# Kernel tuning notes

Hardware: AMD Instinct MI355X
Metric: run time of the kernel (lower is better)

Reference implementation:

```python
import jax, jax.numpy as jnp
import numpy as np

N, C, H, W = 64, 128, 32, 32
EPS = 1e-5


def _layernorm_chw(x, w, b):
    # LayerNorm over normalized_shape=(C,H,W): last 3 dims
    mu = jnp.mean(x, axis=(1, 2, 3), keepdims=True)
    var = jnp.var(x, axis=(1, 2, 3), keepdims=True)
    return (x - mu) * jax.lax.rsqrt(var + EPS) * w[None] + b[None]


def _conv1x1(x, w, b):
    # x: [N,C,H,W], w: [Cout,Cin], b: [Cout]
    return jnp.einsum('oc,nchw->nohw', w, x) + b[None, :, None, None]


def setup_inputs() -> dict:
    key = jax.random.key(0)
    ks = jax.random.split(key, 12)
    d = {
        'query': jax.random.normal(ks[0], (N, C, H, W), jnp.float32),
        'key': jax.random.normal(ks[1], (N, C, H, W), jnp.float32),
        'value': jax.random.normal(ks[2], (N, C, H, W), jnp.float32),
        'ln1_w': jnp.ones((C, H, W), jnp.float32),
        'ln1_b': jnp.zeros((C, H, W), jnp.float32),
        'ln2_w': jnp.ones((C, H, W), jnp.float32),
        'ln2_b': jnp.zeros((C, H, W), jnp.float32),
        'ln3_w': jnp.ones((C, H, W), jnp.float32),
        'ln3_b': jnp.zeros((C, H, W), jnp.float32),
        'wq': jax.random.normal(ks[3], (C, C), jnp.float32) / np.sqrt(C),
        'bq': jnp.zeros((C,), jnp.float32),
        'wk': jax.random.normal(ks[4], (C, C), jnp.float32) / np.sqrt(C),
        'bk': jnp.zeros((C,), jnp.float32),
        'wv': jax.random.normal(ks[5], (C, C), jnp.float32) / np.sqrt(C),
        'bv': jnp.zeros((C,), jnp.float32),
    }
    return d


def reference(query, key, value, ln1_w, ln1_b, ln2_w, ln2_b, ln3_w, ln3_b,
              wq, bq, wk, bk, wv, bv):
    qn = _layernorm_chw(query, ln1_w, ln1_b)  # residual uses normalized query
    kn = _layernorm_chw(key, ln2_w, ln2_b)
    vn = _layernorm_chw(value, ln3_w, ln3_b)
    q = _conv1x1(qn, wq, bq).reshape(N, C, H * W)
    k = _conv1x1(kn, wk, bk).reshape(N, C, H * W)
    v = _conv1x1(vn, wv, bv).reshape(N, C, H * W)
    # attention[n,i,j] = sum_c k[n,c,i] q[n,c,j] / sqrt(C); softmax over i (dim=1)
    attn = jnp.einsum('nci,ncj->nij', k, q) / jnp.sqrt(jnp.float32(C))
    attn = jax.nn.softmax(attn, axis=1)
    out = jnp.einsum('nci,nij->ncj', v, attn).reshape(N, C, H, W)
    x = qn + out
    return x.reshape(N, -1)  # flatten(start_dim=1)
```

## Files before the change

kernel.cpp:

```cpp
#include <hip/hip_runtime.h>


#define NS 64
#define CD 128
#define SD 1024
#define MEL (CD*SD)
#define SCALE 0.08838834764831845f

typedef __attribute__((ext_vector_type(4))) float floatx4;
typedef __attribute__((ext_vector_type(8))) short short8;
typedef __attribute__((ext_vector_type(4))) short short4v;

typedef __attribute__((address_space(1))) const void global_cvoid;
typedef __attribute__((address_space(3))) void lds_void;

__device__ __forceinline__ void gl16(const void* g, void* l) {
  __builtin_amdgcn_global_load_lds((global_cvoid*)g, (lds_void*)l, 16, 0, 0);
}
__device__ __forceinline__ unsigned short f2bf(float f) {
  union { float f; unsigned int i; } v; v.f = f;
  unsigned int i = v.i;
  return (unsigned short)((i + 0x7fffu + ((i >> 16) & 1u)) >> 16);
}
__device__ __forceinline__ unsigned int pkbf(float lo, float hi) {
  unsigned int r;
  asm("v_cvt_pk_bf16_f32 %0, %1, %2" : "=v"(r) : "v"(lo), "v"(hi));
  return r;
}
__device__ __forceinline__ short8 ld8_bf16(const float* __restrict__ p) {
  floatx4 a = *(const floatx4*)p;
  floatx4 b = *(const floatx4*)(p + 4);
  short8 r;
  r[0] = (short)f2bf(a[0]); r[1] = (short)f2bf(a[1]);
  r[2] = (short)f2bf(a[2]); r[3] = (short)f2bf(a[3]);
  r[4] = (short)f2bf(b[0]); r[5] = (short)f2bf(b[1]);
  r[6] = (short)f2bf(b[2]); r[7] = (short)f2bf(b[3]);
  return r;
}
__device__ __forceinline__ floatx4 mfma16(short8 a, short8 b, floatx4 c) {
  return __builtin_amdgcn_mfma_f32_16x16x32_bf16(a, b, c, 0, 0, 0);
}

__global__ __launch_bounds__(256) void stats_kernel(
    const float* __restrict__ q, const float* __restrict__ k,
    const float* __restrict__ v, float* __restrict__ sums)
{
  int b = blockIdx.x;
  int tn = b >> 3, part = b & 7;
  int t = tn >> 6;
  const float* x = (t == 0 ? q : (t == 1 ? k : v))
                 + (size_t)(tn & 63) * MEL + part * (MEL / 8);
  float s1 = 0.f, s2 = 0.f;
#pragma unroll
  for (int it = 0; it < 16; ++it) {
    floatx4 u = *(const floatx4*)(x + it * 1024 + threadIdx.x * 4);
#pragma unroll
    for (int j = 0; j < 4; ++j) { float f = u[j]; s1 += f; s2 += f * f; }
  }
#pragma unroll
  for (int off = 32; off; off >>= 1) {
    s1 += __shfl_xor(s1, off, 64);
    s2 += __shfl_xor(s2, off, 64);
  }
  if ((threadIdx.x & 63) == 0) {
    atomicAdd(&sums[tn], s1);
    atomicAdd(&sums[192 + tn], s2);
  }
}

__global__ __launch_bounds__(512, 4) void proj_kernel(
  const float* __restrict__ k, const float* __restrict__ v,
  const float* __restrict__ l2w, const float* __restrict__ l2b,
  const float* __restrict__ l3w, const float* __restrict__ l3b,
  const float* __restrict__ wk, const float* __restrict__ bk,
  const float* __restrict__ wv, const float* __restrict__ bv,
  const float* __restrict__ sums,
  unsigned short* __restrict__ kT, unsigned short* __restrict__ vN)
{
  int n  = blockIdx.x, t = blockIdx.y, st = blockIdx.z;
  const float* x  = (t == 0 ? k : v) + (size_t)n * MEL;
  const float* lw = (t == 0 ? l2w : l3w);
  const float* lb = (t == 0 ? l2b : l3b);
  const float* W  = (t == 0 ? wk : wv);
  const float* Bs = (t == 0 ? bk : bv);

  float mu  = sums[(t + 1) * 64 + n] * (1.f / MEL);
  float var = sums[192 + (t + 1) * 64 + n] * (1.f / MEL) - mu * mu;
  float rs  = rsqrtf(var + 1e-5f);
  float a_ln = rs, b_ln = -mu * rs;

  __shared__ __align__(16) unsigned short Xt[128 * 136];

  int tid = threadIdx.x;
  int cb = tid & 15, sb = (tid >> 4) & 15, half = tid >> 8;
  int s0 = st * 128;

  unsigned int w32[8][2];
#pragma unroll
  for (int pr = 0; pr < 2; ++pr) {
    int c0 = cb * 8 + half * 4 + pr * 2;
    const float* xp0 = x  + (size_t)c0 * SD + s0 + sb * 8;
    const float* wp0 = lw + (size_t)c0 * SD + s0 + sb * 8;
    const float* bp0 = lb + (size_t)c0 * SD + s0 + sb * 8;
    float xv0[8], xv1[8], wv0[8], wv1[8], bv0[8], bv1[8];
    *(floatx4*)xv0 = *(const floatx4*)xp0;       *(floatx4*)(xv0+4) = *(const floatx4*)(xp0+4);
    *(floatx4*)xv1 = *(const floatx4*)(xp0+SD);  *(floatx4*)(xv1+4) = *(const floatx4*)(xp0+SD+4);
    *(floatx4*)wv0 = *(const floatx4*)wp0;       *(floatx4*)(wv0+4) = *(const floatx4*)(wp0+4);
    *(floatx4*)wv1 = *(const floatx4*)(wp0+SD);  *(floatx4*)(wv1+4) = *(const floatx4*)(wp0+SD+4);
    *(floatx4*)bv0 = *(const floatx4*)bp0;       *(floatx4*)(bv0+4) = *(const floatx4*)(bp0+4);
    *(floatx4*)bv1 = *(const floatx4*)(bp0+SD);  *(floatx4*)(bv1+4) = *(const floatx4*)(bp0+SD+4);
#pragma unroll
    for (int js = 0; js < 8; ++js) {
      unsigned int lo = f2bf((xv0[js] * a_ln + b_ln) * wv0[js] + bv0[js]);
      unsigned int hi = f2bf((xv1[js] * a_ln + b_ln) * wv1[js] + bv1[js]);
      w32[js][pr] = lo | (hi << 16);
    }
  }
#pragma unroll
  for (int js = 0; js < 8; ++js) {
    unsigned int* d = (unsigned int*)&Xt[(sb * 8 + js) * 136 + cb * 8 + half * 4];
    d[0] = w32[js][0]; d[1] = w32[js][1];
  }
  __syncthreads();

  int lane = tid & 63, w = tid >> 6;
  int quad = lane >> 4, l16 = lane & 15;

  short8 Af[4];
#pragma unroll
  for (int kk = 0; kk < 4; ++kk)
    Af[kk] = ld8_bf16(W + (w * 16 + l16) * CD + kk * 32 + quad * 8);

  floatx4 acc[8];
  floatx4 zz = {0.f, 0.f, 0.f, 0.f};
#pragma unroll
  for (int nb = 0; nb < 8; ++nb) acc[nb] = zz;
#pragma unroll
  for (int kk = 0; kk < 4; ++kk)
#pragma unroll
    for (int nb = 0; nb < 8; ++nb) {
      short8 Bf = *(const short8*)&Xt[(nb * 16 + l16) * 136 + kk * 32 + quad * 8];
      acc[nb] = mfma16(Af[kk], Bf, acc[nb]);
    }

  float bsv[4];
#pragma unroll
  for (int r = 0; r < 4; ++r) bsv[r] = Bs[w * 16 + quad * 4 + r];

  if (t == 0) {
#pragma unroll
    for (int nb = 0; nb < 8; ++nb) {
      short4v pk;
#pragma unroll
      for (int r = 0; r < 4; ++r) pk[r] = (short)f2bf(acc[nb][r] + bsv[r]);
      size_t g = (size_t)n * MEL + (size_t)(s0 + nb * 16 + l16) * CD + w * 16 + quad * 4;
      *(short4v*)(kT + g) = pk;
    }
  } else {
#pragma unroll
    for (int nb = 0; nb < 8; ++nb)
#pragma unroll
      for (int r = 0; r < 4; ++r) {
        size_t g = (size_t)n * MEL + (size_t)(w * 16 + quad * 4 + r) * SD + s0 + nb * 16 + l16;
        vN[g] = f2bf(acc[nb][r] + bsv[r]);
      }
  }
}

__device__ __forceinline__ void stage_tile(
    const unsigned short* __restrict__ kbase0,
    const unsigned short* __restrict__ vbase0,
    char* smem, int ti, int buf, int w, int lane)
{
  const unsigned short* kb = kbase0 + (size_t)ti * 64 * CD;
  char* KD = smem + buf * 16384;
  char* VD = smem + 32768 + buf * 16384;
#pragma unroll
  for (int it = 0; it < 4; ++it) {
    int nch = w * 256 + it * 64 + lane;
    int i = nch >> 4, cc = nch & 15;
    int csrc = (cc & 8) | ((cc & 7) ^ (i & 7));
    gl16(kb + i * CD + csrc * 8, KD + (w * 256 + it * 64) * 16);
  }
#pragma unroll
  for (int it = 0; it < 4; ++it) {
    int nch = w * 256 + it * 64 + lane;
    int c = nch >> 3, ci = nch & 7;
    int isrc = ci ^ (c & 7);
    gl16(vbase0 + (size_t)c * SD + ti * 64 + isrc * 8, VD + (w * 256 + it * 64) * 16);
  }
}

__global__ __launch_bounds__(256, 2) void attn_kernel(
  const float* __restrict__ qraw, const float* __restrict__ l1w,
  const float* __restrict__ l1b, const float* __restrict__ wq,
  const float* __restrict__ bq,
  const unsigned short* __restrict__ kT, const unsigned short* __restrict__ vN,
  const float* __restrict__ sums, float* __restrict__ out)
{
  int n = blockIdx.x, jt = blockIdx.y;
  int j0 = jt * 128;

  __shared__ __align__(16) char smem[65536];
  unsigned short* Xt = (unsigned short*)smem;

  int tid = threadIdx.x, lane = tid & 63, w = tid >> 6;
  int quad = lane >> 4, l16 = lane & 15;

  float mu  = sums[n] * (1.f / MEL);
  float var = sums[192 + n] * (1.f / MEL) - mu * mu;
  float rsd = rsqrtf(var + 1e-5f);
  float a_ln = rsd, b_ln = -mu * rsd;
  const float* qb = qraw + (size_t)n * MEL;

  {
    int cb = tid & 15, sb = tid >> 4;
    unsigned int w32[8][4];
#pragma unroll
    for (int pr = 0; pr < 4; ++pr) {
      int c0 = cb * 8 + pr * 2;
      const float* xp0 = qb  + (size_t)c0 * SD + j0 + sb * 8;
      const float* wp0 = l1w + (size_t)c0 * SD + j0 + sb * 8;
      const float* bp0 = l1b + (size_t)c0 * SD + j0 + sb * 8;
      float xv0[8], xv1[8], wv0[8], wv1[8], bv0[8], bv1[8];
      *(floatx4*)xv0 = *(const floatx4*)xp0;       *(floatx4*)(xv0+4) = *(const floatx4*)(xp0+4);
      *(floatx4*)xv1 = *(const floatx4*)(xp0+SD);  *(floatx4*)(xv1+4) = *(const floatx4*)(xp0+SD+4);
      *(floatx4*)wv0 = *(const floatx4*)wp0;       *(floatx4*)(wv0+4) = *(const floatx4*)(wp0+4);
      *(floatx4*)wv1 = *(const floatx4*)(wp0+SD);  *(floatx4*)(wv1+4) = *(const floatx4*)(wp0+SD+4);
      *(floatx4*)bv0 = *(const floatx4*)bp0;       *(floatx4*)(bv0+4) = *(const floatx4*)(bp0+4);
      *(floatx4*)bv1 = *(const floatx4*)(bp0+SD);  *(floatx4*)(bv1+4) = *(const floatx4*)(bp0+SD+4);
#pragma unroll
      for (int js = 0; js < 8; ++js) {
        unsigned int lo = f2bf((xv0[js] * a_ln + b_ln) * wv0[js] + bv0[js]);
        unsigned int hi = f2bf((xv1[js] * a_ln + b_ln) * wv1[js] + bv1[js]);
        w32[js][pr] = lo | (hi << 16);
      }
    }
#pragma unroll
    for (int js = 0; js < 8; ++js)
      *(floatx4*)&Xt[(sb * 8 + js) * 136 + cb * 8] = *(floatx4*)w32[js];
  }
  __syncthreads();

  floatx4 zz = {0.f, 0.f, 0.f, 0.f};
  {
    short8 Af[2][4];
#pragma unroll
    for (int mi = 0; mi < 2; ++mi)
#pragma unroll
      for (int kk = 0; kk < 4; ++kk)
        Af[mi][kk] = ld8_bf16(wq + ((w * 2 + mi) * 16 + l16) * CD + kk * 32 + quad * 8);
    floatx4 accq[2][8];
#pragma unroll
    for (int mi = 0; mi < 2; ++mi)
#pragma unroll
      for (int nb = 0; nb < 8; ++nb) accq[mi][nb] = zz;
#pragma unroll
    for (int kk = 0; kk < 4; ++kk)
#pragma unroll
      for (int nb = 0; nb < 8; ++nb) {
        short8 Bf = *(const short8*)&Xt[(nb * 16 + l16) * 136 + kk * 32 + quad * 8];
        accq[0][nb] = mfma16(Af[0][kk], Bf, accq[0][nb]);
        accq[1][nb] = mfma16(Af[1][kk], Bf, accq[1][nb]);
      }
    __syncthreads();
    float bqs[2][4];
#pragma unroll
    for (int mi = 0; mi < 2; ++mi)
#pragma unroll
      for (int r = 0; r < 4; ++r) bqs[mi][r] = bq[(w * 2 + mi) * 16 + quad * 4 + r];
#pragma unroll
    for (int mi = 0; mi < 2; ++mi)
#pragma unroll
      for (int nb = 0; nb < 8; ++nb) {
        short4v pk;
#pragma unroll
        for (int r = 0; r < 4; ++r) pk[r] = (short)f2bf(accq[mi][nb][r] + bqs[mi][r]);
        *(short4v*)&Xt[(nb * 16 + l16) * 136 + (w * 2 + mi) * 16 + quad * 4] = pk;
      }
  }
  __syncthreads();

  short8 Qf[2][4];
#pragma unroll
  for (int nt = 0; nt < 2; ++nt)
#pragma unroll
    for (int kk = 0; kk < 4; ++kk)
      Qf[nt][kk] = *(const short8*)&Xt[((w * 2 + nt) * 16 + l16) * 136 + kk * 32 + quad * 8];
  __syncthreads();

  floatx4 Oc[8][2];
#pragma unroll
  for (int mt = 0; mt < 8; ++mt) { Oc[mt][0] = zz; Oc[mt][1] = zz; }
  float lsum[2] = {0.f, 0.f};

  const unsigned short* kbase0 = kT + (size_t)n * MEL;
  const unsigned short* vbase0 = vN + (size_t)n * MEL;

  int idx0 = l16 + ((quad & 1) << 5);
  int idx1 = idx0 + 16;
  bool hiq = quad >= 2;

  stage_tile(kbase0, vbase0, smem, 0, 0, w, lane);

  for (int itile = 0; itile < 16; ++itile) {
    int buf = itile & 1;
    __syncthreads();
    if (itile < 15) stage_tile(kbase0, vbase0, smem, itile + 1, buf ^ 1, w, lane);

    const unsigned short* Ks = (const unsigned short*)(smem + buf * 16384);
    const unsigned short* Vs = (const unsigned short*)(smem + 32768 + buf * 16384);

    floatx4 Sa[4][2];
#pragma unroll
    for (int mt = 0; mt < 4; ++mt) { Sa[mt][0] = zz; Sa[mt][1] = zz; }
    __builtin_amdgcn_s_setprio(1);
#pragma unroll
    for (int kk = 0; kk < 4; ++kk)
#pragma unroll
      for (int mt = 0; mt < 4; ++mt) {
        short8 Kf = *(const short8*)&Ks[(mt * 16 + l16) * 128 + (((kk * 4 + quad) ^ (l16 & 7)) * 8)];
        Sa[mt][0] = mfma16(Kf, Qf[0][kk], Sa[mt][0]);
        Sa[mt][1] = mfma16(Kf, Qf[1][kk], Sa[mt][1]);
      }
    __builtin_amdgcn_s_setprio(0);

    unsigned int pp[2][4][2];
#pragma unroll
    for (int nt = 0; nt < 2; ++nt)
#pragma unroll
      for (int mt = 0; mt < 4; ++mt) {
        float p0 = __expf(Sa[mt][nt][0] * SCALE);
        float p1 = __expf(Sa[mt][nt][1] * SCALE);
        float p2 = __expf(Sa[mt][nt][2] * SCALE);
        float p3 = __expf(Sa[mt][nt][3] * SCALE);
        lsum[nt] += (p0 + p1) + (p2 + p3);
        pp[nt][mt][0] = pkbf(p0, p1);
        pp[nt][mt][1] = pkbf(p2, p3);
      }

#pragma unroll
    for (int kk = 0; kk < 2; ++kk) {
      short8 Pf[2];
#pragma unroll
      for (int nt = 0; nt < 2; ++nt) {
        unsigned int d0a = (unsigned int)__shfl((int)pp[nt][2*kk  ][0], idx0, 64);
        unsigned int d0b = (unsigned int)__shfl((int)pp[nt][2*kk+1][0], idx0, 64);
        unsigned int d1a = (unsigned int)__shfl((int)pp[nt][2*kk  ][1], idx0, 64);
        unsigned int d1b = (unsigned int)__shfl((int)pp[nt][2*kk+1][1], idx0, 64);
        unsigned int d2a = (unsigned int)__shfl((int)pp[nt][2*kk  ][0], idx1, 64);
        unsigned int d2b = (unsigned int)__shfl((int)pp[nt][2*kk+1][0], idx1, 64);
        unsigned int d3a = (unsigned int)__shfl((int)pp[nt][2*kk  ][1], idx1, 64);
        unsigned int d3b = (unsigned int)__shfl((int)pp[nt][2*kk+1][1], idx1, 64);
        union { unsigned int u[4]; short8 s; } pu;
        pu.u[0] = hiq ? d0b : d0a;
        pu.u[1] = hiq ? d1b : d1a;
        pu.u[2] = hiq ? d2b : d2a;
        pu.u[3] = hiq ? d3b : d3a;
        Pf[nt] = pu.s;
      }
      __builtin_amdgcn_s_setprio(1);
#pragma unroll
      for (int mt = 0; mt < 8; ++mt) {
        short8 Vf = *(const short8*)&Vs[(mt * 16 + l16) * 64 + (((kk * 4 + quad) ^ (l16 & 7)) * 8)];
        Oc[mt][0] = mfma16(Vf, Pf[0], Oc[mt][0]);
        Oc[mt][1] = mfma16(Vf, Pf[1], Oc[mt][1]);
      }
      __builtin_amdgcn_s_setprio(0);
    }
  }

#pragma unroll
  for (int nt = 0; nt < 2; ++nt) {
    lsum[nt] += __shfl_xor(lsum[nt], 16, 64);
    lsum[nt] += __shfl_xor(lsum[nt], 32, 64);
  }
  float linv0 = 1.f / lsum[0], linv1 = 1.f / lsum[1];
  int jA = (w * 2) * 16 + l16, jB = jA + 16;

#pragma unroll
  for (int mt = 0; mt < 8; ++mt) {
#pragma unroll
    for (int r = 0; r < 4; ++r) {
      int c = mt * 16 + quad * 4 + r;
      const float* qp = qb  + (size_t)c * SD + j0;
      const float* wp = l1w + (size_t)c * SD + j0;
      const float* bp = l1b + (size_t)c * SD + j0;
      float* op = out + (size_t)n * MEL + (size_t)c * SD + j0;
      float qnA = (qp[jA] * a_ln + b_ln) * wp[jA] + bp[jA];
      float qnB = (qp[jB] * a_ln + b_ln) * wp[jB] + bp[jB];
      op[jA] = Oc[mt][0][r] * linv0 + qnA;
      op[jB] = Oc[mt][1][r] * linv1 + qnB;
    }
  }
}

extern "C" void kernel_launch(void* const* d_in, const int* in_sizes, int n_in,
                              void* d_out, int out_size, void* d_ws, size_t ws_size,
                              hipStream_t stream)
{
  const float* q   = (const float*)d_in[0];
  const float* k   = (const float*)d_in[1];
  const float* v   = (const float*)d_in[2];
  const float* l1w = (const float*)d_in[3];
  const float* l1b = (const float*)d_in[4];
  const float* l2w = (const float*)d_in[5];
  const float* l2b = (const float*)d_in[6];
  const float* l3w = (const float*)d_in[7];
  const float* l3b = (const float*)d_in[8];
  const float* wq  = (const float*)d_in[9];
  const float* bq  = (const float*)d_in[10];
  const float* wk  = (const float*)d_in[11];
  const float* bk  = (const float*)d_in[12];
  const float* wv  = (const float*)d_in[13];
  const float* bv  = (const float*)d_in[14];

  char* ws = (char*)d_ws;
  float* sums = (float*)ws;
  unsigned short* kT = (unsigned short*)(ws + 4096);
  unsigned short* vN = kT + (size_t)NS * MEL;

  hipMemsetAsync(sums, 0, 384 * sizeof(float), stream);
  stats_kernel<<<1536, 256, 0, stream>>>(q, k, v, sums);
  proj_kernel<<<dim3(64, 2, 8), 512, 0, stream>>>(k, v, l2w, l2b, l3w, l3b,
      wk, bk, wv, bv, sums, kT, vN);
  attn_kernel<<<dim3(64, 8), 256, 0, stream>>>(q, l1w, l1b, wq, bq, kT, vN,
      sums, (float*)d_out);
}
```

Baseline: 268.5 us.

## Split attention work across 8 waves with one 16-query tile per wave

The attention kernel now launches 512 threads (8 waves) per block instead of 256, and each wave owns a single 16-column query tile rather than two. The Q projection, the K/V tile staging, the softmax and the PV accumulation are all re-partitioned to match. Per-wave register use drops, which allows higher occupancy and more latency hiding. In exchange, each K/V fragment read from LDS is reused by fewer MFMAs, and the launch bound asks for 4 blocks of 512 threads per CU, which with 64KB of LDS per block may not be reachable.

Result: faster. 262.3 us (-2.3%).

```diff
diff --git a/kernel.cpp b/kernel.cpp
--- a/kernel.cpp
+++ b/kernel.cpp
@@ -176,22 +176,22 @@
   char* KD = smem + buf * 16384;
   char* VD = smem + 32768 + buf * 16384;
 #pragma unroll
-  for (int it = 0; it < 4; ++it) {
-    int nch = w * 256 + it * 64 + lane;
+  for (int it = 0; it < 2; ++it) {
+    int nch = w * 128 + it * 64 + lane;
     int i = nch >> 4, cc = nch & 15;
     int csrc = (cc & 8) | ((cc & 7) ^ (i & 7));
-    gl16(kb + i * CD + csrc * 8, KD + (w * 256 + it * 64) * 16);
-  }
-#pragma unroll
-  for (int it = 0; it < 4; ++it) {
-    int nch = w * 256 + it * 64 + lane;
+    gl16(kb + i * CD + csrc * 8, KD + nch * 16);
+  }
+#pragma unroll
+  for (int it = 0; it < 2; ++it) {
+    int nch = w * 128 + it * 64 + lane;
     int c = nch >> 3, ci = nch & 7;
     int isrc = ci ^ (c & 7);
-    gl16(vbase0 + (size_t)c * SD + ti * 64 + isrc * 8, VD + (w * 256 + it * 64) * 16);
-  }
-}
-
-__global__ __launch_bounds__(256, 2) void attn_kernel(
+    gl16(vbase0 + (size_t)c * SD + ti * 64 + isrc * 8, VD + nch * 16);
+  }
+}
+
+__global__ __launch_bounds__(512, 4) void attn_kernel(
   const float* __restrict__ qraw, const float* __restrict__ l1w,
   const float* __restrict__ l1b, const float* __restrict__ wq,
   const float* __restrict__ bq,
@@ -214,11 +214,11 @@
   const float* qb = qraw + (size_t)n * MEL;
 
   {
-    int cb = tid & 15, sb = tid >> 4;
-    unsigned int w32[8][4];
-#pragma unroll
-    for (int pr = 0; pr < 4; ++pr) {
-      int c0 = cb * 8 + pr * 2;
+    int cb = tid & 15, sb = (tid >> 4) & 15, half = tid >> 8;
+    unsigned int w32[8][2];
+#pragma unroll
+    for (int pr = 0; pr < 2; ++pr) {
+      int c0 = cb * 8 + half * 4 + pr * 2;
       const float* xp0 = qb  + (size_t)c0 * SD + j0 + sb * 8;
       const float* wp0 = l1w + (size_t)c0 * SD + j0 + sb * 8;
       const float* bp0 = l1b + (size_t)c0 * SD + j0 + sb * 8;
@@ -237,62 +237,53 @@
       }
     }
 #pragma unroll
-    for (int js = 0; js < 8; ++js)
-      *(floatx4*)&Xt[(sb * 8 + js) * 136 + cb * 8] = *(floatx4*)w32[js];
+    for (int js = 0; js < 8; ++js) {
+      unsigned int* d = (unsigned int*)&Xt[(sb * 8 + js) * 136 + cb * 8 + half * 4];
+      d[0] = w32[js][0]; d[1] = w32[js][1];
+    }
   }
   __syncthreads();
 
   floatx4 zz = {0.f, 0.f, 0.f, 0.f};
   {
-    short8 Af[2][4];
-#pragma unroll
-    for (int mi = 0; mi < 2; ++mi)
-#pragma unroll
-      for (int kk = 0; kk < 4; ++kk)
-        Af[mi][kk] = ld8_bf16(wq + ((w * 2 + mi) * 16 + l16) * CD + kk * 32 + quad * 8);
-    floatx4 accq[2][8];
-#pragma unroll
-    for (int mi = 0; mi < 2; ++mi)
-#pragma unroll
-      for (int nb = 0; nb < 8; ++nb) accq[mi][nb] = zz;
+    short8 Af[4];
+#pragma unroll
+    for (int kk = 0; kk < 4; ++kk)
+      Af[kk] = ld8_bf16(wq + (w * 16 + l16) * CD + kk * 32 + quad * 8);
+    floatx4 accq[8];
+#pragma unroll
+    for (int nb = 0; nb < 8; ++nb) accq[nb] = zz;
 #pragma unroll
     for (int kk = 0; kk < 4; ++kk)
 #pragma unroll
       for (int nb = 0; nb < 8; ++nb) {
         short8 Bf = *(const short8*)&Xt[(nb * 16 + l16) * 136 + kk * 32 + quad * 8];
-        accq[0][nb] = mfma16(Af[0][kk], Bf, accq[0][nb]);
-        accq[1][nb] = mfma16(Af[1][kk], Bf, accq[1][nb]);
+        accq[nb] = mfma16(Af[kk], Bf, accq[nb]);
       }
     __syncthreads();
-    float bqs[2][4];
-#pragma unroll
-    for (int mi = 0; mi < 2; ++mi)
-#pragma unroll
-      for (int r = 0; r < 4; ++r) bqs[mi][r] = bq[(w * 2 + mi) * 16 + quad * 4 + r];
-#pragma unroll
-    for (int mi = 0; mi < 2; ++mi)
-#pragma unroll
-      for (int nb = 0; nb < 8; ++nb) {
-        short4v pk;
-#pragma unroll
-        for (int r = 0; r < 4; ++r) pk[r] = (short)f2bf(accq[mi][nb][r] + bqs[mi][r]);
-        *(short4v*)&Xt[(nb * 16 + l16) * 136 + (w * 2 + mi) * 16 + quad * 4] = pk;
-      }
+    float bqs[4];
+#pragma unroll
+    for (int r = 0; r < 4; ++r) bqs[r] = bq[w * 16 + quad * 4 + r];
+#pragma unroll
+    for (int nb = 0; nb < 8; ++nb) {
+      short4v pk;
+#pragma unroll
+      for (int r = 0; r < 4; ++r) pk[r] = (short)f2bf(accq[nb][r] + bqs[r]);
+      *(short4v*)&Xt[(nb * 16 + l16) * 136 + w * 16 + quad * 4] = pk;
+    }
   }
   __syncthreads();
 
-  short8 Qf[2][4];
-#pragma unroll
-  for (int nt = 0; nt < 2; ++nt)
-#pragma unroll
-    for (int kk = 0; kk < 4; ++kk)
-      Qf[nt][kk] = *(const short8*)&Xt[((w * 2 + nt) * 16 + l16) * 136 + kk * 32 + quad * 8];
+  short8 Qf[4];
+#pragma unroll
+  for (int kk = 0; kk < 4; ++kk)
+    Qf[kk] = *(const short8*)&Xt[(w * 16 + l16) * 136 + kk * 32 + quad * 8];
   __syncthreads();
 
-  floatx4 Oc[8][2];
-#pragma unroll
-  for (int mt = 0; mt < 8; ++mt) { Oc[mt][0] = zz; Oc[mt][1] = zz; }
-  float lsum[2] = {0.f, 0.f};
+  floatx4 Oc[8];
+#pragma unroll
+  for (int mt = 0; mt < 8; ++mt) Oc[mt] = zz;
+  float lsum = 0.f;
 
   const unsigned short* kbase0 = kT + (size_t)n * MEL;
   const unsigned short* vbase0 = vN + (size_t)n * MEL;
@@ -311,86 +302,70 @@
     const unsigned short* Ks = (const unsigned short*)(smem + buf * 16384);
     const unsigned short* Vs = (const unsigned short*)(smem + 32768 + buf * 16384);
 
-    floatx4 Sa[4][2];
-#pragma unroll
-    for (int mt = 0; mt < 4; ++mt) { Sa[mt][0] = zz; Sa[mt][1] = zz; }
+    floatx4 Sa[4];
+#pragma unroll
+    for (int mt = 0; mt < 4; ++mt) Sa[mt] = zz;
     __builtin_amdgcn_s_setprio(1);
 #pragma unroll
     for (int kk = 0; kk < 4; ++kk)
 #pragma unroll
       for (int mt = 0; mt < 4; ++mt) {
         short8 Kf = *(const short8*)&Ks[(mt * 16 + l16) * 128 + (((kk * 4 + quad) ^ (l16 & 7)) * 8)];
-        Sa[mt][0] = mfma16(Kf, Qf[0][kk], Sa[mt][0]);
-        Sa[mt][1] = mfma16(Kf, Qf[1][kk], Sa[mt][1]);
+        Sa[mt] = mfma16(Kf, Qf[kk], Sa[mt]);
       }
     __builtin_amdgcn_s_setprio(0);
 
-    unsigned int pp[2][4][2];
-#pragma unroll
-    for (int nt = 0; nt < 2; ++nt)
-#pragma unroll
-      for (int mt = 0; mt < 4; ++mt) {
-        float p0 = __expf(Sa[mt][nt][0] * SCALE);
-        float p1 = __expf(Sa[mt][nt][1] * SCALE);
-        float p2 = __expf(Sa[mt][nt][2] * SCALE);
-        float p3 = __expf(Sa[mt][nt][3] * SCALE);
-        lsum[nt] += (p0 + p1) + (p2 + p3);
-        pp[nt][mt][0] = pkbf(p0, p1);
-        pp[nt][mt][1] = pkbf(p2, p3);
-      }
+    unsigned int pp[4][2];
+#pragma unroll
+    for (int mt = 0; mt < 4; ++mt) {
+      float p0 = __expf(Sa[mt][0] * SCALE);
+      float p1 = __expf(Sa[mt][1] * SCALE);
+      float p2 = __expf(Sa[mt][2] * SCALE);
+      float p3 = __expf(Sa[mt][3] * SCALE);
+      lsum += (p0 + p1) + (p2 + p3);
+      pp[mt][0] = pkbf(p0, p1);
+      pp[mt][1] = pkbf(p2, p3);
+    }
 
 #pragma unroll
     for (int kk = 0; kk < 2; ++kk) {
-      short8 Pf[2];
-#pragma unroll
-      for (int nt = 0; nt < 2; ++nt) {
-        unsigned int d0a = (unsigned int)__shfl((int)pp[nt][2*kk  ][0], idx0, 64);
-        unsigned int d0b = (unsigned int)__shfl((int)pp[nt][2*kk+1][0], idx0, 64);
-        unsigned int d1a = (unsigned int)__shfl((int)pp[nt][2*kk  ][1], idx0, 64);
-        unsigned int d1b = (unsigned int)__shfl((int)pp[nt][2*kk+1][1], idx0, 64);
-        unsigned int d2a = (unsigned int)__shfl((int)pp[nt][2*kk  ][0], idx1, 64);
-        unsigned int d2b = (unsigned int)__shfl((int)pp[nt][2*kk+1][0], idx1, 64);
-        unsigned int d3a = (unsigned int)__shfl((int)pp[nt][2*kk  ][1], idx1, 64);
-        unsigned int d3b = (unsigned int)__shfl((int)pp[nt][2*kk+1][1], idx1, 64);
-        union { unsigned int u[4]; short8 s; } pu;
-        pu.u[0] = hiq ? d0b : d0a;
-        pu.u[1] = hiq ? d1b : d1a;
-        pu.u[2] = hiq ? d2b : d2a;
-        pu.u[3] = hiq ? d3b : d3a;
-        Pf[nt] = pu.s;
-      }
+      unsigned int d0a = (unsigned int)__shfl((int)pp[2*kk  ][0], idx0, 64);
+      unsigned int d0b = (unsigned int)__shfl((int)pp[2*kk+1][0], idx0, 64);
+      unsigned int d1a = (unsigned int)__shfl((int)pp[2*kk  ][1], idx0, 64);
+      unsigned int d1b = (unsigned int)__shfl((int)pp[2*kk+1][1], idx0, 64);
+      unsigned int d2a = (unsigned int)__shfl((int)pp[2*kk  ][0], idx1, 64);
+      unsigned int d2b = (unsigned int)__shfl((int)pp[2*kk+1][0], idx1, 64);
+      unsigned int d3a = (unsigned int)__shfl((int)pp[2*kk  ][1], idx1, 64);
+      unsigned int d3b = (unsigned int)__shfl((int)pp[2*kk+1][1], idx1, 64);
+      union { unsigned int u[4]; short8 s; } pu;
+      pu.u[0] = hiq ? d0b : d0a;
+      pu.u[1] = hiq ? d1b : d1a;
+      pu.u[2] = hiq ? d2b : d2a;
+      pu.u[3] = hiq ? d3b : d3a;
+      short8 Pf = pu.s;
       __builtin_amdgcn_s_setprio(1);
 #pragma unroll
       for (int mt = 0; mt < 8; ++mt) {
         short8 Vf = *(const short8*)&Vs[(mt * 16 + l16) * 64 + (((kk * 4 + quad) ^ (l16 & 7)) * 8)];
-        Oc[mt][0] = mfma16(Vf, Pf[0], Oc[mt][0]);
-        Oc[mt][1] = mfma16(Vf, Pf[1], Oc[mt][1]);
+        Oc[mt] = mfma16(Vf, Pf, Oc[mt]);
       }
       __builtin_amdgcn_s_setprio(0);
     }
   }
 
-#pragma unroll
-  for (int nt = 0; nt < 2; ++nt) {
-    lsum[nt] += __shfl_xor(lsum[nt], 16, 64);
-    lsum[nt] += __shfl_xor(lsum[nt], 32, 64);
-  }
-  float linv0 = 1.f / lsum[0], linv1 = 1.f / lsum[1];
-  int jA = (w * 2) * 16 + l16, jB = jA + 16;
+  lsum += __shfl_xor(lsum, 16, 64);
+  lsum += __shfl_xor(lsum, 32, 64);
+  float linv = 1.f / lsum;
+  int j = j0 + w * 16 + l16;
 
 #pragma unroll
   for (int mt = 0; mt < 8; ++mt) {
 #pragma unroll
     for (int r = 0; r < 4; ++r) {
       int c = mt * 16 + quad * 4 + r;
-      const float* qp = qb  + (size_t)c * SD + j0;
-      const float* wp = l1w + (size_t)c * SD + j0;
-      const float* bp = l1b + (size_t)c * SD + j0;
-      float* op = out + (size_t)n * MEL + (size_t)c * SD + j0;
-      float qnA = (qp[jA] * a_ln + b_ln) * wp[jA] + bp[jA];
-      float qnB = (qp[jB] * a_ln + b_ln) * wp[jB] + bp[jB];
-      op[jA] = Oc[mt][0][r] * linv0 + qnA;
-      op[jB] = Oc[mt][1][r] * linv1 + qnB;
+      const float* qp = qb  + (size_t)c * SD;
+      float qn = (qp[j] * a_ln + b_ln) * l1w[(size_t)c * SD + j] + l1b[(size_t)c * SD + j];
+      out[(size_t)n * MEL + (size_t)c * SD + j] = Oc[mt][r] * linv + qn;
     }
   }
 }
@@ -424,6 +399,6 @@
   stats_kernel<<<1536, 256, 0, stream>>>(q, k, v, sums);
   proj_kernel<<<dim3(64, 2, 8), 512, 0, stream>>>(k, v, l2w, l2b, l3w, l3b,
       wk, bk, wv, bv, sums, kT, vN);
-  attn_kernel<<<dim3(64, 8), 256, 0, stream>>>(q, l1w, l1b, wq, bq, kT, vN,
+  attn_kernel<<<dim3(64, 8), 512, 0, stream>>>(q, l1w, l1b, wq, bq, kT, vN,
       sums, (float*)d_out);
 }
```
